# Kernel tuning notes

Measured on AMD Instinct MI355X. Metric: run time of the kernel, lower is better.

The kernel has to match this reference:

```python
import jax, jax.numpy as jnp
import numpy as np

N = 50000
E = 800000
F_IN = 128
H = 8        # heads
C = 32       # hidden_channels per head
HC = H * C   # 256
NEG_SLOPE = 0.2


def setup_inputs() -> dict:
    key = jax.random.key(0)
    ks = jax.random.split(key, 16)
    s = 0.1
    return {
        'x': jax.random.normal(ks[0], (N, F_IN), jnp.float32),
        'edge_index': jax.random.randint(ks[1], (2, E), 0, N, jnp.int64),
        'edge_weights': jax.random.uniform(ks[2], (E,), jnp.float32),
        'W1': jax.random.normal(ks[3], (F_IN, HC), jnp.float32) * s,
        'att_src1': jax.random.normal(ks[4], (H, C), jnp.float32) * s,
        'att_dst1': jax.random.normal(ks[5], (H, C), jnp.float32) * s,
        'b1': jnp.zeros((HC,), jnp.float32),
        'W2': jax.random.normal(ks[6], (HC, HC), jnp.float32) * s,
        'att_src2': jax.random.normal(ks[7], (H, C), jnp.float32) * s,
        'att_dst2': jax.random.normal(ks[8], (H, C), jnp.float32) * s,
        'b2': jnp.zeros((HC,), jnp.float32),
        'We': jax.random.normal(ks[9], (HC, 1), jnp.float32) * s,
        'be': jnp.zeros((1,), jnp.float32),
        'Wn': jax.random.normal(ks[10], (HC, 1), jnp.float32) * s,
        'bn': jnp.zeros((1,), jnp.float32),
    }


def gat_conv(x, src, dst, W, att_src, att_dst, bias):
    """PyG GATConv (concat=True, eval mode, self-loops already in src/dst)."""
    n = x.shape[0]
    h = (x @ W).reshape(n, H, C)                      # [N,H,C]
    a_s = jnp.sum(h * att_src, axis=-1)               # [N,H]
    a_d = jnp.sum(h * att_dst, axis=-1)               # [N,H]
    e = jax.nn.leaky_relu(a_s[src] + a_d[dst], NEG_SLOPE)  # [E',H]
    m = jax.ops.segment_max(e, dst, num_segments=n)   # segment softmax over dst
    ex = jnp.exp(e - m[dst])
    denom = jax.ops.segment_sum(ex, dst, num_segments=n)
    alpha = ex / (denom[dst] + 1e-16)                 # [E',H]
    out = jax.ops.segment_sum(alpha[..., None] * h[src], dst, num_segments=n)
    return out.reshape(n, HC) + bias


def reference(x, edge_index, edge_weights, W1, att_src1, att_dst1, b1,
              W2, att_src2, att_dst2, b2, We, be, Wn, bn):
    src0, dst0 = edge_index[0], edge_index[1]
    loops = jnp.arange(N, dtype=src0.dtype)
    src = jnp.concatenate([src0, loops])
    dst = jnp.concatenate([dst0, loops])
    # edge_weights is passed to GATConv as edge_attr but unused (edge_dim=None)
    h = jax.nn.relu(gat_conv(x, src, dst, W1, att_src1, att_dst1, b1))
    h = jax.nn.relu(gat_conv(h, src, dst, W2, att_src2, att_dst2, b2))
    edge_pred = (h[src0] * h[dst0]) @ We + be          # [E,1]
    node_pred = h @ Wn + bn                            # [N,1]
    return (edge_pred, node_pred)
```

## Files before the change

### kernel.cpp

```cpp
#include <hip/hip_runtime.h>
#include <hip/hip_bf16.h>

#define NN 50000
#define NE 800000
#define FIN 128
#define HC 256
#define NEG_SLOPE 0.2f

#define GEMM_BLOCKS 1564
#define NSB 3321
#define NB_ZERO 196
#define NB_X 6250
#define NB_W1 128
#define NB_W2 256

typedef short bf16x8 __attribute__((ext_vector_type(8)));
typedef float f32x4 __attribute__((ext_vector_type(4)));

__device__ __forceinline__ unsigned short f2bf(float f) {
  unsigned u = __float_as_uint(f);
  u += 0x7fff + ((u >> 16) & 1);
  return (unsigned short)(u >> 16);
}
__device__ __forceinline__ float bf2f(unsigned short s) {
  return __uint_as_float((unsigned)s << 16);
}
__device__ __forceinline__ float bflo(unsigned u) { return __uint_as_float(u << 16); }
__device__ __forceinline__ float bfhi(unsigned u) { return __uint_as_float(u & 0xffff0000u); }

__global__ __launch_bounds__(256) void prep_kernel(
    const float* __restrict__ X, unsigned short* __restrict__ Xh,
    const float* __restrict__ W1, unsigned short* __restrict__ W1th,
    unsigned short* __restrict__ W1tl, const float* __restrict__ W2,
    unsigned short* __restrict__ W2th, unsigned short* __restrict__ W2tl,
    int* __restrict__ counts, int* __restrict__ tmp) {
  int b = blockIdx.x, t = threadIdx.x;
  if (b < NB_ZERO) {
    int i = b * 256 + t;
    if (i < NN) { counts[i] = 0; tmp[i] = 0; }
  } else if (b < NB_ZERO + NB_X) {
    int i = (b - NB_ZERO) * 256 + t;
    float4 v = ((const float4*)X)[i];
    ushort4 h;
    h.x = f2bf(v.x); h.y = f2bf(v.y); h.z = f2bf(v.z); h.w = f2bf(v.w);
    ((ushort4*)Xh)[i] = h;
  } else if (b < NB_ZERO + NB_X + NB_W1) {
    int j = (b - NB_ZERO - NB_X) * 256 + t;
    int n = j >> 7, k = j & 127;
    float v = W1[k * HC + n];
    unsigned short h = f2bf(v);
    W1th[j] = h;
    W1tl[j] = f2bf(v - bf2f(h));
  } else {
    int j = (b - NB_ZERO - NB_X - NB_W1) * 256 + t;
    int n = j >> 8, k = j & 255;
    float v = W2[k * HC + n];
    unsigned short h = f2bf(v);
    W2th[j] = h;
    W2tl[j] = f2bf(v - bf2f(h));
  }
}

__global__ __launch_bounds__(256) void gemm_coef(
    const unsigned short* __restrict__ A, const unsigned short* __restrict__ Bth,
    const unsigned short* __restrict__ Btl, const float* __restrict__ att_s,
    const float* __restrict__ att_d, unsigned short* __restrict__ Cb,
    float* __restrict__ a_s, float* __restrict__ a_d, int M, int K,
    const int* __restrict__ ei, const int* __restrict__ rowptr,
    int* __restrict__ tmpc, int2* __restrict__ ce) {
  __shared__ unsigned short sA[64 * 40];
  __shared__ unsigned short sBh[128 * 40];
  __shared__ unsigned short sBl[128 * 40];
  __shared__ float sCS[64][4];
  __shared__ float sCD[64][4];

  int bid = blockIdx.x, t = threadIdx.x;
  if (bid >= GEMM_BLOCKS) {
    int e = (bid - GEMM_BLOCKS) * 256 + t;
    if (e < NE + NN) {
      int s, d, id;
      if (e < NE) { s = ei[e]; d = ei[NE + e]; id = e; }
      else { s = d = e - NE; id = -1; }
      int pos = rowptr[d] + atomicAdd(&tmpc[d], 1);
      ce[pos] = make_int2(s, id);
    }
    return;
  }

  int w = t >> 6, lane = t & 63;
  int quad = lane >> 4, lrow = lane & 15;
  int m0 = (bid >> 1) * 64, n0 = (bid & 1) * 128;
  int rm = (w & 1) * 32, cn = (w >> 1) * 64;

  f32x4 acc[2][4] = {};

  for (int k0 = 0; k0 < K; k0 += 32) {
    {
      int row = t >> 2, q = t & 3;
      int gm = m0 + row;
      if (gm >= M) gm = M - 1;
      *(uint4*)(sA + row * 40 + q * 8) = *(const uint4*)(A + (size_t)gm * K + k0 + q * 8);
    }
#pragma unroll
    for (int i = 0; i < 2; ++i) {
      int idx = t + i * 256;
      int row = idx >> 2, q = idx & 3;
      size_t gb = (size_t)(n0 + row) * K + k0 + q * 8;
      *(uint4*)(sBh + row * 40 + q * 8) = *(const uint4*)(Bth + gb);
      *(uint4*)(sBl + row * 40 + q * 8) = *(const uint4*)(Btl + gb);
    }
    __syncthreads();

    bf16x8 fa[2];
#pragma unroll
    for (int mi = 0; mi < 2; ++mi)
      fa[mi] = *(const bf16x8*)(sA + (rm + mi * 16 + lrow) * 40 + quad * 8);
#pragma unroll
    for (int ni = 0; ni < 4; ++ni) {
      bf16x8 fbh = *(const bf16x8*)(sBh + (cn + ni * 16 + lrow) * 40 + quad * 8);
      bf16x8 fbl = *(const bf16x8*)(sBl + (cn + ni * 16 + lrow) * 40 + quad * 8);
#pragma unroll
      for (int mi = 0; mi < 2; ++mi) {
        acc[mi][ni] = __builtin_amdgcn_mfma_f32_16x16x32_bf16(fa[mi], fbh, acc[mi][ni], 0, 0, 0);
        acc[mi][ni] = __builtin_amdgcn_mfma_f32_16x16x32_bf16(fa[mi], fbl, acc[mi][ni], 0, 0, 0);
      }
    }
    __syncthreads();
  }

  float vs[4], vd[4];
#pragma unroll
  for (int ni = 0; ni < 4; ++ni) {
    int gn = n0 + cn + ni * 16 + lrow;
    vs[ni] = att_s[gn];
    vd[ni] = att_d[gn];
  }
  int h4e = cn >> 5;

#pragma unroll
  for (int mi = 0; mi < 2; ++mi) {
#pragma unroll
    for (int r = 0; r < 4; ++r) {
      int lr = rm + mi * 16 + quad * 4 + r;
      int gm = m0 + lr;
      if (gm < M) {
#pragma unroll
        for (int ni = 0; ni < 4; ++ni) {
          int gn = n0 + cn + ni * 16 + lrow;
          Cb[(size_t)gm * HC + gn] = f2bf(acc[mi][ni][r]);
        }
      }
      float pse = acc[mi][0][r] * vs[0] + acc[mi][1][r] * vs[1];
      float pso = acc[mi][2][r] * vs[2] + acc[mi][3][r] * vs[3];
      float pde = acc[mi][0][r] * vd[0] + acc[mi][1][r] * vd[1];
      float pdo = acc[mi][2][r] * vd[2] + acc[mi][3][r] * vd[3];
#pragma unroll
      for (int off = 1; off <= 8; off <<= 1) {
        pse += __shfl_xor(pse, off);
        pso += __shfl_xor(pso, off);
        pde += __shfl_xor(pde, off);
        pdo += __shfl_xor(pdo, off);
      }
      if (lrow == 0) {
        sCS[lr][h4e] = pse;
        sCS[lr][h4e + 1] = pso;
        sCD[lr][h4e] = pde;
        sCD[lr][h4e + 1] = pdo;
      }
    }
  }
  __syncthreads();
  if (t < 64) {
    int gm = m0 + t;
    if (gm < M) {
      int o = (n0 >> 5);
      *(float4*)(a_s + (size_t)gm * 8 + o) = *(const float4*)&sCS[t][0];
      *(float4*)(a_d + (size_t)gm * 8 + o) = *(const float4*)&sCD[t][0];
    }
  }
}

__global__ void hist_kernel(const int* __restrict__ ei, int* __restrict__ counts) {
  int e = blockIdx.x * 256 + threadIdx.x;
  if (e < NE) atomicAdd(&counts[ei[NE + e]], 1);
}

__global__ void scan1(const int* __restrict__ counts, int* __restrict__ scanbuf,
                      int* __restrict__ bsum) {
  __shared__ int sd[256];
  int t = threadIdx.x;
  int i = blockIdx.x * 256 + t;
  int v = (i < NN) ? counts[i] + 1 : 0;
  sd[t] = v;
  __syncthreads();
#pragma unroll
  for (int off = 1; off < 256; off <<= 1) {
    int x = (t >= off) ? sd[t - off] : 0;
    __syncthreads();
    sd[t] += x;
    __syncthreads();
  }
  if (i < NN) scanbuf[i] = sd[t];
  if (t == 255) bsum[blockIdx.x] = sd[255];
}

__global__ void scan2(const int* __restrict__ bsum, int* __restrict__ boff, int nb) {
  __shared__ int sd[256];
  int t = threadIdx.x;
  int v = (t < nb) ? bsum[t] : 0;
  sd[t] = v;
  __syncthreads();
#pragma unroll
  for (int off = 1; off < 256; off <<= 1) {
    int x = (t >= off) ? sd[t - off] : 0;
    __syncthreads();
    sd[t] += x;
    __syncthreads();
  }
  if (t < nb) boff[t] = sd[t] - v;
}

__global__ void scan3(const int* __restrict__ scanbuf, const int* __restrict__ boff,
                      int* __restrict__ rowptr) {
  int i = blockIdx.x * 256 + threadIdx.x;
  if (i < NN) rowptr[i + 1] = scanbuf[i] + boff[blockIdx.x];
  if (i == 0) rowptr[0] = 0;
}

__global__ __launch_bounds__(256) void agg_kernel(
    const unsigned short* __restrict__ htb, const float* __restrict__ a_s,
    const float* __restrict__ a_d, const int* __restrict__ rowptr,
    const int2* __restrict__ ce, const float* __restrict__ bias,
    unsigned short* __restrict__ outb,
    const float* __restrict__ Wn, const float* __restrict__ bn,
    float* __restrict__ outn) {
  int d = blockIdx.x * 8 + (threadIdx.x >> 5);
  if (d >= NN) return;
  int l = threadIdx.x & 31;
  int hh = l >> 2;
  float adh = a_d[d * 8 + hh];
  int r0 = rowptr[d], r1 = rowptr[d + 1];
  float denom = 0.f;
  float4 acc0 = {0.f, 0.f, 0.f, 0.f};
  float4 acc1 = {0.f, 0.f, 0.f, 0.f};
  for (int r = r0; r < r1; r += 4) {
    int s[4];
    float as_[4];
    uint4 q[4];
    bool ok[4];
#pragma unroll
    for (int j = 0; j < 4; ++j) {
      int rj = r + j;
      ok[j] = rj < r1;
      rj = ok[j] ? rj : r1 - 1;
      s[j] = ce[rj].x;
    }
#pragma unroll
    for (int j = 0; j < 4; ++j) {
      as_[j] = a_s[s[j] * 8 + hh];
      q[j] = ((const uint4*)(htb + (size_t)s[j] * HC))[l];
    }
#pragma unroll
    for (int j = 0; j < 4; ++j) {
      float e = as_[j] + adh;
      e = e > 0.f ? e : NEG_SLOPE * e;
      float w = ok[j] ? __expf(e) : 0.f;
      denom += w;
      acc0.x += w * bflo(q[j].x);
      acc0.y += w * bfhi(q[j].x);
      acc0.z += w * bflo(q[j].y);
      acc0.w += w * bfhi(q[j].y);
      acc1.x += w * bflo(q[j].z);
      acc1.y += w * bfhi(q[j].z);
      acc1.z += w * bflo(q[j].w);
      acc1.w += w * bfhi(q[j].w);
    }
  }
  float dv = 1.f / denom;
  float4 b0 = *(const float4*)(bias + l * 8);
  float4 b1 = *(const float4*)(bias + l * 8 + 4);
  float4 o0, o1;
  o0.x = fmaxf(fmaf(acc0.x, dv, b0.x), 0.f);
  o0.y = fmaxf(fmaf(acc0.y, dv, b0.y), 0.f);
  o0.z = fmaxf(fmaf(acc0.z, dv, b0.z), 0.f);
  o0.w = fmaxf(fmaf(acc0.w, dv, b0.w), 0.f);
  o1.x = fmaxf(fmaf(acc1.x, dv, b1.x), 0.f);
  o1.y = fmaxf(fmaf(acc1.y, dv, b1.y), 0.f);
  o1.z = fmaxf(fmaf(acc1.z, dv, b1.z), 0.f);
  o1.w = fmaxf(fmaf(acc1.w, dv, b1.w), 0.f);
  uint4 pb;
  pb.x = (unsigned)f2bf(o0.x) | ((unsigned)f2bf(o0.y) << 16);
  pb.y = (unsigned)f2bf(o0.z) | ((unsigned)f2bf(o0.w) << 16);
  pb.z = (unsigned)f2bf(o1.x) | ((unsigned)f2bf(o1.y) << 16);
  pb.w = (unsigned)f2bf(o1.z) | ((unsigned)f2bf(o1.w) << 16);
  ((uint4*)(outb + (size_t)d * HC))[l] = pb;
  if (outn) {
    const float4* wnp = (const float4*)(Wn + l * 8);
    float4 w0 = wnp[0], w1 = wnp[1];
    float p = o0.x * w0.x + o0.y * w0.y + o0.z * w0.z + o0.w * w0.w +
              o1.x * w1.x + o1.y * w1.y + o1.z * w1.z + o1.w * w1.w;
#pragma unroll
    for (int off = 1; off <= 16; off <<= 1) p += __shfl_xor(p, off);
    if (l == 0) outn[d] = p + bn[0];
  }
}

__global__ __launch_bounds__(256) void edge_pred_kernel(
    const unsigned short* __restrict__ h2b, const int* __restrict__ rowptr,
    const int2* __restrict__ ce, const float* __restrict__ We,
    const float* __restrict__ be, float* __restrict__ out) {
  int d = blockIdx.x * 4 + (threadIdx.x >> 6);
  if (d >= NN) return;
  int lane = threadIdx.x & 63;
  int g = lane >> 4, l = lane & 15;
  float b = be[0];

  const uint4* rowd = (const uint4*)(h2b + (size_t)d * HC + l * 16);
  uint4 qd0 = rowd[0], qd1 = rowd[1];
  float wd[16];
  {
    const float4* wep = (const float4*)(We + l * 16);
    float4 w0 = wep[0], w1 = wep[1], w2 = wep[2], w3 = wep[3];
    wd[0] = bflo(qd0.x) * w0.x;  wd[1] = bfhi(qd0.x) * w0.y;
    wd[2] = bflo(qd0.y) * w0.z;  wd[3] = bfhi(qd0.y) * w0.w;
    wd[4] = bflo(qd0.z) * w1.x;  wd[5] = bfhi(qd0.z) * w1.y;
    wd[6] = bflo(qd0.w) * w1.z;  wd[7] = bfhi(qd0.w) * w1.w;
    wd[8] = bflo(qd1.x) * w2.x;  wd[9] = bfhi(qd1.x) * w2.y;
    wd[10] = bflo(qd1.y) * w2.z; wd[11] = bfhi(qd1.y) * w2.w;
    wd[12] = bflo(qd1.z) * w3.x; wd[13] = bfhi(qd1.z) * w3.y;
    wd[14] = bflo(qd1.w) * w3.z; wd[15] = bfhi(qd1.w) * w3.w;
  }

  int r0 = rowptr[d], r1 = rowptr[d + 1];
  for (int r = r0; r < r1; r += 8) {
    int rr0 = r + g, rr1 = r + 4 + g;
    int s0 = 0, id0 = -1, s1 = 0, id1 = -1;
    if (rr0 < r1) { int2 p = ce[rr0]; s0 = p.x; id0 = p.y; }
    if (rr1 < r1) { int2 p = ce[rr1]; s1 = p.x; id1 = p.y; }
    const uint4* ra = (const uint4*)(h2b + (size_t)s0 * HC + l * 16);
    const uint4* rb = (const uint4*)(h2b + (size_t)s1 * HC + l * 16);
    uint4 a0 = ra[0], a1 = ra[1];
    uint4 c0 = rb[0], c1 = rb[1];
    float p0 = bflo(a0.x) * wd[0] + bfhi(a0.x) * wd[1] + bflo(a0.y) * wd[2] +
               bfhi(a0.y) * wd[3] + bflo(a0.z) * wd[4] + bfhi(a0.z) * wd[5] +
               bflo(a0.w) * wd[6] + bfhi(a0.w) * wd[7] + bflo(a1.x) * wd[8] +
               bfhi(a1.x) * wd[9] + bflo(a1.y) * wd[10] + bfhi(a1.y) * wd[11] +
               bflo(a1.z) * wd[12] + bfhi(a1.z) * wd[13] + bflo(a1.w) * wd[14] +
               bfhi(a1.w) * wd[15];
    float p1 = bflo(c0.x) * wd[0] + bfhi(c0.x) * wd[1] + bflo(c0.y) * wd[2] +
               bfhi(c0.y) * wd[3] + bflo(c0.z) * wd[4] + bfhi(c0.z) * wd[5] +
               bflo(c0.w) * wd[6] + bfhi(c0.w) * wd[7] + bflo(c1.x) * wd[8] +
               bfhi(c1.x) * wd[9] + bflo(c1.y) * wd[10] + bfhi(c1.y) * wd[11] +
               bflo(c1.z) * wd[12] + bfhi(c1.z) * wd[13] + bflo(c1.w) * wd[14] +
               bfhi(c1.w) * wd[15];
#pragma unroll
    for (int off = 1; off <= 8; off <<= 1) {
      p0 += __shfl_xor(p0, off);
      p1 += __shfl_xor(p1, off);
    }
    if (l == 0) {
      if (id0 >= 0) out[id0] = p0 + b;
      if (id1 >= 0) out[id1] = p1 + b;
    }
  }
}

extern "C" void kernel_launch(void* const* d_in, const int* in_sizes, int n_in,
                              void* d_out, int out_size, void* d_ws, size_t ws_size,
                              hipStream_t stream) {
  const float* x  = (const float*)d_in[0];
  const int* ei   = (const int*)d_in[1];
  const float* W1 = (const float*)d_in[3];
  const float* as1 = (const float*)d_in[4];
  const float* ad1 = (const float*)d_in[5];
  const float* b1 = (const float*)d_in[6];
  const float* W2 = (const float*)d_in[7];
  const float* as2 = (const float*)d_in[8];
  const float* ad2 = (const float*)d_in[9];
  const float* b2 = (const float*)d_in[10];
  const float* We = (const float*)d_in[11];
  const float* be = (const float*)d_in[12];
  const float* Wn = (const float*)d_in[13];
  const float* bn = (const float*)d_in[14];
  float* out = (float*)d_out;

  char* wsp = (char*)d_ws;
  auto alloc = [&](size_t bytes) {
    char* p = wsp;
    wsp += (bytes + 255) & ~(size_t)255;
    return p;
  };
  unsigned short* hbA = (unsigned short*)alloc((size_t)NN * HC * 2);
  unsigned short* h1b = (unsigned short*)alloc((size_t)NN * HC * 2);
  unsigned short* hbB = (unsigned short*)alloc((size_t)NN * HC * 2);
  float* a_s = (float*)alloc((size_t)NN * 8 * 4);
  float* a_d = (float*)alloc((size_t)NN * 8 * 4);
  int* rowptr = (int*)alloc((size_t)(NN + 1) * 4);
  int2* ce = (int2*)alloc((size_t)(NE + NN + 8) * 8);
  int* counts = (int*)alloc((size_t)NN * 4);
  int* tmp = (int*)alloc((size_t)NN * 4);
  int* scanbuf = (int*)alloc((size_t)NN * 4);
  int* bsum = (int*)alloc(256 * 4);
  int* boff = (int*)alloc(256 * 4);
  unsigned short* W1th = (unsigned short*)alloc((size_t)FIN * HC * 2);
  unsigned short* W1tl = (unsigned short*)alloc((size_t)FIN * HC * 2);
  unsigned short* W2th = (unsigned short*)alloc((size_t)HC * HC * 2);
  unsigned short* W2tl = (unsigned short*)alloc((size_t)HC * HC * 2);

  unsigned short* xh = h1b;

  const int NB = (NN + 255) / 256;

  prep_kernel<<<NB_ZERO + NB_X + NB_W1 + NB_W2, 256, 0, stream>>>(
      x, xh, W1, W1th, W1tl, W2, W2th, W2tl, counts, tmp);
  hist_kernel<<<(NE + 255) / 256, 256, 0, stream>>>(ei, counts);
  scan1<<<NB, 256, 0, stream>>>(counts, scanbuf, bsum);
  scan2<<<1, 256, 0, stream>>>(bsum, boff, NB);
  scan3<<<NB, 256, 0, stream>>>(scanbuf, boff, rowptr);

  gemm_coef<<<GEMM_BLOCKS + NSB, 256, 0, stream>>>(
      xh, W1th, W1tl, as1, ad1, hbA, a_s, a_d, NN, FIN, ei, rowptr, tmp, ce);
  agg_kernel<<<NN / 8, 256, 0, stream>>>(hbA, a_s, a_d, rowptr, ce, b1, h1b,
                                         (const float*)nullptr, (const float*)nullptr,
                                         (float*)nullptr);

  gemm_coef<<<GEMM_BLOCKS, 256, 0, stream>>>(
      h1b, W2th, W2tl, as2, ad2, hbA, a_s, a_d, NN, HC,
      (const int*)nullptr, rowptr, tmp, ce);
  agg_kernel<<<NN / 8, 256, 0, stream>>>(hbA, a_s, a_d, rowptr, ce, b2, hbB,
                                         Wn, bn, out + NE);

  edge_pred_kernel<<<NN / 4, 256, 0, stream>>>(hbB, rowptr, ce, We, be, out);
}
```

Before: 435.7 us.

## Prefetch next GEMM K-tile into registers and dispatch scatter blocks first

The GEMM main loop now loads the next K-slice of A and both split-bf16 B halves into registers while MFMAs run on the current shared-memory tile, replacing the load-then-sync pattern. The edge-scatter (CSR fill) blocks are moved to the front of the grid so they dispatch before the GEMM blocks, selected by a new runtime parameter. The aim is to hide global-load latency in the GEMM and overlap the atomic scatter with the GEMM tail. The cost is more registers per thread and a changed synchronisation pattern in the loop.

```diff
diff --git a/kernel.cpp b/kernel.cpp
--- a/kernel.cpp
+++ b/kernel.cpp
@@ -67,7 +67,7 @@
     const float* __restrict__ att_d, unsigned short* __restrict__ Cb,
     float* __restrict__ a_s, float* __restrict__ a_d, int M, int K,
     const int* __restrict__ ei, const int* __restrict__ rowptr,
-    int* __restrict__ tmpc, int2* __restrict__ ce) {
+    int* __restrict__ tmpc, int2* __restrict__ ce, int scat) {
   __shared__ unsigned short sA[64 * 40];
   __shared__ unsigned short sBh[128 * 40];
   __shared__ unsigned short sBl[128 * 40];
@@ -75,8 +75,8 @@
   __shared__ float sCD[64][4];
 
   int bid = blockIdx.x, t = threadIdx.x;
-  if (bid >= GEMM_BLOCKS) {
-    int e = (bid - GEMM_BLOCKS) * 256 + t;
+  if (bid < scat) {
+    int e = bid * 256 + t;
     if (e < NE + NN) {
       int s, d, id;
       if (e < NE) { s = ei[e]; d = ei[NE + e]; id = e; }
@@ -86,30 +86,48 @@
     }
     return;
   }
+  int gid = bid - scat;
 
   int w = t >> 6, lane = t & 63;
   int quad = lane >> 4, lrow = lane & 15;
-  int m0 = (bid >> 1) * 64, n0 = (bid & 1) * 128;
+  int m0 = (gid >> 1) * 64, n0 = (gid & 1) * 128;
   int rm = (w & 1) * 32, cn = (w >> 1) * 64;
 
+  int rowA = t >> 2, qA = t & 3;
+  int gmA = m0 + rowA; if (gmA >= M) gmA = M - 1;
+  const unsigned short* pA = A + (size_t)gmA * K + qA * 8;
+  int rowB0 = t >> 2;
+  int rowB1 = (t + 256) >> 2;
+  const unsigned short* pBh0 = Bth + (size_t)(n0 + rowB0) * K + qA * 8;
+  const unsigned short* pBh1 = Bth + (size_t)(n0 + rowB1) * K + qA * 8;
+  const unsigned short* pBl0 = Btl + (size_t)(n0 + rowB0) * K + qA * 8;
+  const unsigned short* pBl1 = Btl + (size_t)(n0 + rowB1) * K + qA * 8;
+
+  uint4 ra  = *(const uint4*)(pA);
+  uint4 rh0 = *(const uint4*)(pBh0);
+  uint4 rh1 = *(const uint4*)(pBh1);
+  uint4 rl0 = *(const uint4*)(pBl0);
+  uint4 rl1 = *(const uint4*)(pBl1);
+
   f32x4 acc[2][4] = {};
 
   for (int k0 = 0; k0 < K; k0 += 32) {
-    {
-      int row = t >> 2, q = t & 3;
-      int gm = m0 + row;
-      if (gm >= M) gm = M - 1;
-      *(uint4*)(sA + row * 40 + q * 8) = *(const uint4*)(A + (size_t)gm * K + k0 + q * 8);
-    }
-#pragma unroll
-    for (int i = 0; i < 2; ++i) {
-      int idx = t + i * 256;
-      int row = idx >> 2, q = idx & 3;
-      size_t gb = (size_t)(n0 + row) * K + k0 + q * 8;
-      *(uint4*)(sBh + row * 40 + q * 8) = *(const uint4*)(Bth + gb);
-      *(uint4*)(sBl + row * 40 + q * 8) = *(const uint4*)(Btl + gb);
-    }
-    __syncthreads();
+    __syncthreads();
+    *(uint4*)(sA + rowA * 40 + qA * 8) = ra;
+    *(uint4*)(sBh + rowB0 * 40 + qA * 8) = rh0;
+    *(uint4*)(sBh + rowB1 * 40 + qA * 8) = rh1;
+    *(uint4*)(sBl + rowB0 * 40 + qA * 8) = rl0;
+    *(uint4*)(sBl + rowB1 * 40 + qA * 8) = rl1;
+    __syncthreads();
+
+    int k1 = k0 + 32;
+    if (k1 < K) {
+      ra  = *(const uint4*)(pA + k1);
+      rh0 = *(const uint4*)(pBh0 + k1);
+      rh1 = *(const uint4*)(pBh1 + k1);
+      rl0 = *(const uint4*)(pBl0 + k1);
+      rl1 = *(const uint4*)(pBl1 + k1);
+    }
 
     bf16x8 fa[2];
 #pragma unroll
@@ -125,7 +143,6 @@
         acc[mi][ni] = __builtin_amdgcn_mfma_f32_16x16x32_bf16(fa[mi], fbl, acc[mi][ni], 0, 0, 0);
       }
     }
-    __syncthreads();
   }
 
   float vs[4], vd[4];
@@ -418,15 +435,15 @@
   scan2<<<1, 256, 0, stream>>>(bsum, boff, NB);
   scan3<<<NB, 256, 0, stream>>>(scanbuf, boff, rowptr);
 
-  gemm_coef<<<GEMM_BLOCKS + NSB, 256, 0, stream>>>(
-      xh, W1th, W1tl, as1, ad1, hbA, a_s, a_d, NN, FIN, ei, rowptr, tmp, ce);
+  gemm_coef<<<NSB + GEMM_BLOCKS, 256, 0, stream>>>(
+      xh, W1th, W1tl, as1, ad1, hbA, a_s, a_d, NN, FIN, ei, rowptr, tmp, ce, NSB);
   agg_kernel<<<NN / 8, 256, 0, stream>>>(hbA, a_s, a_d, rowptr, ce, b1, h1b,
                                          (const float*)nullptr, (const float*)nullptr,
                                          (float*)nullptr);
 
   gemm_coef<<<GEMM_BLOCKS, 256, 0, stream>>>(
       h1b, W2th, W2tl, as2, ad2, hbA, a_s, a_d, NN, HC,
-      (const int*)nullptr, rowptr, tmp, ce);
+      (const int*)nullptr, rowptr, tmp, ce, 0);
   agg_kernel<<<NN / 8, 256, 0, stream>>>(hbA, a_s, a_d, rowptr, ce, b2, hbB,
                                          Wn, bn, out + NE);
 
```

Measured after the change: 445.3 us. +2.2%, slower.
